# Kernel tuning notes

Measured on AMD Instinct MI355X. Metric: run time of the kernel, lower is better.

The kernel has to match this reference:

```python
import jax, jax.numpy as jnp
import numpy as np

B = 256
D, H, W = 15, 64, 128    # depth, latitude, longitude of input grid
d, h, w = 5, 16, 32      # grid after AveragePooling3D(3,4,4)
L_DEPTH = (d + 2) * h * w      # 3584
L_LON   = d * h * (w + 2)      # 2720
L_LAT   = d * (h + 2) * w      # 2880


def _local1d(xp, wt, bias):
    # Unshared-weight LocallyConnected1D(filters=1, kernel=3) + relu.
    # xp: (B, L+2) padded sequence; wt: (L, 3); bias: (L,)
    L = wt.shape[0]
    y = (wt[:, 0] * xp[:, 0:L]
         + wt[:, 1] * xp[:, 1:L + 1]
         + wt[:, 2] * xp[:, 2:L + 2]
         + bias)
    return jax.nn.relu(y)


def setup_inputs() -> dict:
    key = jax.random.key(0)
    ks = jax.random.split(key, 7)
    s = 0.1
    return {
        "x": jax.random.normal(ks[0], (B, D, H, W, 1), jnp.float32),
        "w_depth": jax.random.normal(ks[1], (L_DEPTH, 3), jnp.float32) * s,
        "b_depth": jax.random.normal(ks[2], (L_DEPTH,), jnp.float32) * s,
        "w_lon": jax.random.normal(ks[3], (L_LON, 3), jnp.float32) * s,
        "b_lon": jax.random.normal(ks[4], (L_LON,), jnp.float32) * s,
        "w_lat": jax.random.normal(ks[5], (L_LAT, 3), jnp.float32) * s,
        "b_lat": jax.random.normal(ks[6], (L_LAT,), jnp.float32) * s,
    }


def reference(x, w_depth, b_depth, w_lon, b_lon, w_lat, b_lat):
    Bn = x.shape[0]
    # AveragePooling3D(3,4,4): dims divide evenly -> reshape + mean
    xs = x.reshape(Bn, d, 3, h, 4, w, 4, 1).mean(axis=(2, 4, 6))  # (B,d,h,w,1)

    # ---- depth axis: pad depth, permute (3,2,1,4), flatten, local conv ----
    t = jnp.pad(xs, ((0, 0), (1, 1), (0, 0), (0, 0), (0, 0)))     # (B,d+2,h,w,1)
    t = jnp.transpose(t, (0, 3, 2, 1, 4))                         # (B,w,h,d+2,1)
    t = t.reshape(Bn, L_DEPTH)
    t = jnp.pad(t, ((0, 0), (1, 1)))                              # ZeroPadding1D(1)
    t = _local1d(t, w_depth, b_depth)
    t = t.reshape(Bn, w, h, d + 2, 1)
    t = jnp.transpose(t, (0, 3, 2, 1, 4))                         # (B,d+2,h,w,1)
    t = t[:, 1:-1]                                                # crop depth -> (B,d,h,w,1)

    # ---- longitude axis: pad last spatial dim, identity permute ----
    u = jnp.pad(t, ((0, 0), (0, 0), (0, 0), (1, 1), (0, 0)))      # (B,d,h,w+2,1)
    u = u.reshape(Bn, L_LON)
    u = jnp.pad(u, ((0, 0), (1, 1)))
    u = _local1d(u, w_lon, b_lon)
    u = u.reshape(Bn, d, h, w + 2, 1)
    u = u[:, :, :, 1:-1]                                          # (B,d,h,w,1)

    # ---- latitude axis: pad lat, permute (1,3,2,4) ----
    v = jnp.pad(u, ((0, 0), (0, 0), (1, 1), (0, 0), (0, 0)))      # (B,d,h+2,w,1)
    v = jnp.transpose(v, (0, 1, 3, 2, 4))                         # (B,d,w,h+2,1)
    v = v.reshape(Bn, L_LAT)
    v = jnp.pad(v, ((0, 0), (1, 1)))
    v = _local1d(v, w_lat, b_lat)
    v = v.reshape(Bn, d, w, h + 2, 1)
    v = jnp.transpose(v, (0, 1, 3, 2, 4))                         # (B,d,h+2,w,1)
    v = v[:, :, 1:-1]                                             # (B,d,h,w,1)

    # UpSampling3D(3,4,4): nearest-neighbor repeat
    out = jnp.broadcast_to(
        v[:, :, None, :, None, :, None, :],
        (Bn, d, 3, h, 4, w, 4, 1)
    ).reshape(Bn, D, H, W, 1)
    return out
```

## Files before the change

kernel.cpp:

```cpp
#include <hip/hip_runtime.h>


#define NELEM (15 * 64 * 128)
#define NCELL 2560
#define LD    3584
#define LLON  2720

__global__ __launch_bounds__(256) void k_down(const float* __restrict__ x,
                                              float* __restrict__ ds)
{
    const int b  = blockIdx.y;
    const int c  = blockIdx.x * 256 + threadIdx.x;
    const int iw = c & 31;
    const int ih = (c >> 5) & 15;
    const int id = c >> 9;

    const float* p = x + (size_t)b * NELEM + ((id * 3) * 64 + ih * 4) * 128 + iw * 4;
    float s = 0.f;
    #pragma unroll
    for (int dd = 0; dd < 3; ++dd) {
        #pragma unroll
        for (int hh = 0; hh < 4; ++hh) {
            const float4 v = *reinterpret_cast<const float4*>(p + (dd * 64 + hh) * 128);
            s += (v.x + v.y) + (v.z + v.w);
        }
    }
    ds[(size_t)b * NCELL + c] = s * (1.f / 48.f);
}

__device__ __forceinline__ float tf_depth(const float* __restrict__ dsb, int f)
{
    const int k  = f % 7;
    const int q  = f / 7;
    const int ih = q & 15;
    const int iw = q >> 4;
    return (k >= 1 && k <= 5) ? dsb[((k - 1) * 16 + ih) * 32 + iw] : 0.f;
}

__device__ __forceinline__ float t1_val(const float* __restrict__ dsb,
                                        const float* __restrict__ wd,
                                        const float* __restrict__ bd, int l)
{
    const float x0 = (l > 0)      ? tf_depth(dsb, l - 1) : 0.f;
    const float x1 =                tf_depth(dsb, l);
    const float x2 = (l < LD - 1) ? tf_depth(dsb, l + 1) : 0.f;
    return fmaxf(wd[l * 3] * x0 + wd[l * 3 + 1] * x1 + wd[l * 3 + 2] * x2 + bd[l], 0.f);
}

__device__ __forceinline__ float uf_lon(const float* __restrict__ dsb,
                                        const float* __restrict__ wd,
                                        const float* __restrict__ bd, int f)
{
    const int kw  = f % 34;
    const int q   = f / 34;
    const int ih  = q & 15;
    const int dep = q >> 4;
    if (kw < 1 || kw > 32) return 0.f;
    return t1_val(dsb, wd, bd, ((kw - 1) * 16 + ih) * 7 + dep + 1);
}

__global__ __launch_bounds__(256) void k_mid(const float* __restrict__ ds,
                                             const float* __restrict__ wd,
                                             const float* __restrict__ bd,
                                             const float* __restrict__ wl,
                                             const float* __restrict__ bl,
                                             float* __restrict__ u1)
{
    const int b = blockIdx.y;
    const int m = blockIdx.x * 256 + threadIdx.x;
    if (m >= LLON) return;
    const float* dsb = ds + (size_t)b * NCELL;

    const float x0 = (m > 0)        ? uf_lon(dsb, wd, bd, m - 1) : 0.f;
    const float x1 =                  uf_lon(dsb, wd, bd, m);
    const float x2 = (m < LLON - 1) ? uf_lon(dsb, wd, bd, m + 1) : 0.f;
    const float y  = wl[m * 3] * x0 + wl[m * 3 + 1] * x1 + wl[m * 3 + 2] * x2 + bl[m];
    u1[(size_t)b * LLON + m] = fmaxf(y, 0.f);
}

__device__ __forceinline__ float vf_lat(const float* __restrict__ u1b, int f)
{
    const int kh  = f % 18;
    const int q   = f / 18;
    const int iw  = q & 31;
    const int dep = q >> 5;
    return (kh >= 1 && kh <= 16) ? u1b[(dep * 16 + kh - 1) * 34 + iw + 1] : 0.f;
}

__global__ __launch_bounds__(256) void k_vup(const float* __restrict__ u1,
                                             const float* __restrict__ w,
                                             const float* __restrict__ bias,
                                             float* __restrict__ out)
{
    const int b   = blockIdx.y;
    const int c   = blockIdx.x * 256 + threadIdx.x;
    const int iww = c & 31;
    const int ihh = (c >> 5) & 15;
    const int dep = c >> 9;
    const int n   = (dep * 32 + iww) * 18 + ihh + 1;

    const float* u1b = u1 + (size_t)b * LLON;
    const float x0 = vf_lat(u1b, n - 1);
    const float x1 = vf_lat(u1b, n);
    const float x2 = vf_lat(u1b, n + 1);
    const float y  = fmaxf(w[n * 3] * x0 + w[n * 3 + 1] * x1 + w[n * 3 + 2] * x2 + bias[n], 0.f);
    const float4 y4 = make_float4(y, y, y, y);

    float4* ob = reinterpret_cast<float4*>(out + (size_t)b * NELEM);
    #pragma unroll
    for (int dd = 0; dd < 3; ++dd) {
        #pragma unroll
        for (int hh = 0; hh < 4; ++hh) {
            ob[((dep * 3 + dd) * 64 + ihh * 4 + hh) * 32 + iww] = y4;
        }
    }
}

extern "C" void kernel_launch(void* const* d_in, const int* in_sizes, int n_in,
                              void* d_out, int out_size, void* d_ws, size_t ws_size,
                              hipStream_t stream) {
    const float* x       = (const float*)d_in[0];
    const float* w_depth = (const float*)d_in[1];
    const float* b_depth = (const float*)d_in[2];
    const float* w_lon   = (const float*)d_in[3];
    const float* b_lon   = (const float*)d_in[4];
    const float* w_lat   = (const float*)d_in[5];
    const float* b_lat   = (const float*)d_in[6];
    float* out = (float*)d_out;

    const int Bn = in_sizes[0] / NELEM;

    float* ds = (float*)d_ws;
    float* u1 = ds + (size_t)Bn * NCELL;

    k_down<<<dim3(NCELL / 256, Bn), dim3(256), 0, stream>>>(x, ds);
    k_mid <<<dim3((LLON + 255) / 256, Bn), dim3(256), 0, stream>>>(ds, w_depth, b_depth,
                                                                   w_lon, b_lon, u1);
    k_vup <<<dim3(NCELL / 256, Bn), dim3(256), 0, stream>>>(u1, w_lat, b_lat, out);
}
```

Before: 242.0 us.

## Fuse avg-pool downsample into depth/longitude kernel via per-latitude LDS tile

Merges the pooling kernel and the depth+longitude local-conv kernel into one launch. Each block owns one latitude row for one batch, pools the 5x32 cells into shared memory, then computes the 170 longitude outputs for that row straight from LDS. This is valid because the depth and longitude stages never mix latitude rows. It removes one launch and the global round trip of the pooled array. In exchange only 160 and 170 of the 256 threads do work in each phase, and there are fewer, lighter blocks.

```diff
diff --git a/kernel.cpp b/kernel.cpp
--- a/kernel.cpp
+++ b/kernel.cpp
@@ -6,76 +6,76 @@
 #define LD    3584
 #define LLON  2720
 
-__global__ __launch_bounds__(256) void k_down(const float* __restrict__ x,
-                                              float* __restrict__ ds)
-{
-    const int b  = blockIdx.y;
-    const int c  = blockIdx.x * 256 + threadIdx.x;
-    const int iw = c & 31;
-    const int ih = (c >> 5) & 15;
-    const int id = c >> 9;
-
-    const float* p = x + (size_t)b * NELEM + ((id * 3) * 64 + ih * 4) * 128 + iw * 4;
-    float s = 0.f;
-    #pragma unroll
-    for (int dd = 0; dd < 3; ++dd) {
-        #pragma unroll
-        for (int hh = 0; hh < 4; ++hh) {
-            const float4 v = *reinterpret_cast<const float4*>(p + (dd * 64 + hh) * 128);
-            s += (v.x + v.y) + (v.z + v.w);
-        }
-    }
-    ds[(size_t)b * NCELL + c] = s * (1.f / 48.f);
-}
-
-__device__ __forceinline__ float tf_depth(const float* __restrict__ dsb, int f)
+__device__ __forceinline__ float tf_depth_lds(const float* __restrict__ lds, int f)
 {
     const int k  = f % 7;
     const int q  = f / 7;
-    const int ih = q & 15;
     const int iw = q >> 4;
-    return (k >= 1 && k <= 5) ? dsb[((k - 1) * 16 + ih) * 32 + iw] : 0.f;
+    return (k >= 1 && k <= 5) ? lds[(k - 1) * 32 + iw] : 0.f;
 }
 
-__device__ __forceinline__ float t1_val(const float* __restrict__ dsb,
-                                        const float* __restrict__ wd,
-                                        const float* __restrict__ bd, int l)
+__device__ __forceinline__ float t1_val_lds(const float* __restrict__ lds,
+                                            const float* __restrict__ wd,
+                                            const float* __restrict__ bd, int l)
 {
-    const float x0 = (l > 0)      ? tf_depth(dsb, l - 1) : 0.f;
-    const float x1 =                tf_depth(dsb, l);
-    const float x2 = (l < LD - 1) ? tf_depth(dsb, l + 1) : 0.f;
+    const float x0 = tf_depth_lds(lds, l - 1);
+    const float x1 = tf_depth_lds(lds, l);
+    const float x2 = tf_depth_lds(lds, l + 1);
     return fmaxf(wd[l * 3] * x0 + wd[l * 3 + 1] * x1 + wd[l * 3 + 2] * x2 + bd[l], 0.f);
 }
 
-__device__ __forceinline__ float uf_lon(const float* __restrict__ dsb,
-                                        const float* __restrict__ wd,
-                                        const float* __restrict__ bd, int f)
+__device__ __forceinline__ float uf_lon_lds(const float* __restrict__ lds,
+                                            const float* __restrict__ wd,
+                                            const float* __restrict__ bd,
+                                            int f, int ih)
 {
     const int kw  = f % 34;
-    const int q   = f / 34;
-    const int ih  = q & 15;
-    const int dep = q >> 4;
     if (kw < 1 || kw > 32) return 0.f;
-    return t1_val(dsb, wd, bd, ((kw - 1) * 16 + ih) * 7 + dep + 1);
+    const int dep = (f / 34) >> 4;
+    return t1_val_lds(lds, wd, bd, ((kw - 1) * 16 + ih) * 7 + dep + 1);
 }
 
-__global__ __launch_bounds__(256) void k_mid(const float* __restrict__ ds,
-                                             const float* __restrict__ wd,
-                                             const float* __restrict__ bd,
-                                             const float* __restrict__ wl,
-                                             const float* __restrict__ bl,
-                                             float* __restrict__ u1)
+__global__ __launch_bounds__(256) void k_down_mid(const float* __restrict__ x,
+                                                  const float* __restrict__ wd,
+                                                  const float* __restrict__ bd,
+                                                  const float* __restrict__ wl,
+                                                  const float* __restrict__ bl,
+                                                  float* __restrict__ u1)
 {
-    const int b = blockIdx.y;
-    const int m = blockIdx.x * 256 + threadIdx.x;
-    if (m >= LLON) return;
-    const float* dsb = ds + (size_t)b * NCELL;
+    const int b   = blockIdx.y;
+    const int ih  = blockIdx.x;
+    const int tid = threadIdx.x;
 
-    const float x0 = (m > 0)        ? uf_lon(dsb, wd, bd, m - 1) : 0.f;
-    const float x1 =                  uf_lon(dsb, wd, bd, m);
-    const float x2 = (m < LLON - 1) ? uf_lon(dsb, wd, bd, m + 1) : 0.f;
-    const float y  = wl[m * 3] * x0 + wl[m * 3 + 1] * x1 + wl[m * 3 + 2] * x2 + bl[m];
-    u1[(size_t)b * LLON + m] = fmaxf(y, 0.f);
+    __shared__ float ds[5 * 32];
+
+    if (tid < 160) {
+        const int iw = tid & 31;
+        const int id = tid >> 5;
+        const float* p = x + (size_t)b * NELEM + ((id * 3) * 64 + ih * 4) * 128 + iw * 4;
+        float s = 0.f;
+        #pragma unroll
+        for (int dd = 0; dd < 3; ++dd) {
+            #pragma unroll
+            for (int hh = 0; hh < 4; ++hh) {
+                const float4 v = *reinterpret_cast<const float4*>(p + (dd * 64 + hh) * 128);
+                s += (v.x + v.y) + (v.z + v.w);
+            }
+        }
+        ds[id * 32 + iw] = s * (1.f / 48.f);
+    }
+    __syncthreads();
+
+    if (tid < 170) {
+        const int kw  = tid % 34;
+        const int dep = tid / 34;
+        const int m   = (dep * 16 + ih) * 34 + kw;
+
+        const float x0 = (m > 0)        ? uf_lon_lds(ds, wd, bd, m - 1, ih) : 0.f;
+        const float x1 =                  uf_lon_lds(ds, wd, bd, m,     ih);
+        const float x2 = (m < LLON - 1) ? uf_lon_lds(ds, wd, bd, m + 1, ih) : 0.f;
+        const float y  = wl[m * 3] * x0 + wl[m * 3 + 1] * x1 + wl[m * 3 + 2] * x2 + bl[m];
+        u1[(size_t)b * LLON + m] = fmaxf(y, 0.f);
+    }
 }
 
 __device__ __forceinline__ float vf_lat(const float* __restrict__ u1b, int f)
@@ -130,11 +130,9 @@
 
     const int Bn = in_sizes[0] / NELEM;
 
-    float* ds = (float*)d_ws;
-    float* u1 = ds + (size_t)Bn * NCELL;
+    float* u1 = (float*)d_ws;
 
-    k_down<<<dim3(NCELL / 256, Bn), dim3(256), 0, stream>>>(x, ds);
-    k_mid <<<dim3((LLON + 255) / 256, Bn), dim3(256), 0, stream>>>(ds, w_depth, b_depth,
-                                                                   w_lon, b_lon, u1);
-    k_vup <<<dim3(NCELL / 256, Bn), dim3(256), 0, stream>>>(u1, w_lat, b_lat, out);
+    k_down_mid<<<dim3(16, Bn), dim3(256), 0, stream>>>(x, w_depth, b_depth,
+                                                       w_lon, b_lon, u1);
+    k_vup     <<<dim3(NCELL / 256, Bn), dim3(256), 0, stream>>>(u1, w_lat, b_lat, out);
 }
```

New measurement: 231.1 us. -4.5%, faster.

## Fuse depth, longitude and latitude stages into one per-depth-slice kernel

Applied to the files above, without the earlier changes.

Replaces the k_mid and k_vup kernels with a single k_rest kernel. Each block handles one batch item and one depth slice, stages three neighbouring depth slices of the pooled grid in shared memory, computes the depth and longitude local convolutions, keeps the longitude result in LDS, then applies the latitude convolution and writes the upsampled output. This removes one kernel launch, the u1 global round-trip and the recomputation of depth values, at the cost of redundant depth-stencil work across neighbouring iw and two block-level syncs.

```diff
diff --git a/kernel.cpp b/kernel.cpp
--- a/kernel.cpp
+++ b/kernel.cpp
@@ -3,8 +3,6 @@
 
 #define NELEM (15 * 64 * 128)
 #define NCELL 2560
-#define LD    3584
-#define LLON  2720
 
 __global__ __launch_bounds__(256) void k_down(const float* __restrict__ x,
                                               float* __restrict__ ds)
@@ -28,90 +26,76 @@
     ds[(size_t)b * NCELL + c] = s * (1.f / 48.f);
 }
 
-__device__ __forceinline__ float tf_depth(const float* __restrict__ dsb, int f)
-{
-    const int k  = f % 7;
-    const int q  = f / 7;
-    const int ih = q & 15;
-    const int iw = q >> 4;
-    return (k >= 1 && k <= 5) ? dsb[((k - 1) * 16 + ih) * 32 + iw] : 0.f;
-}
-
-__device__ __forceinline__ float t1_val(const float* __restrict__ dsb,
-                                        const float* __restrict__ wd,
-                                        const float* __restrict__ bd, int l)
-{
-    const float x0 = (l > 0)      ? tf_depth(dsb, l - 1) : 0.f;
-    const float x1 =                tf_depth(dsb, l);
-    const float x2 = (l < LD - 1) ? tf_depth(dsb, l + 1) : 0.f;
-    return fmaxf(wd[l * 3] * x0 + wd[l * 3 + 1] * x1 + wd[l * 3 + 2] * x2 + bd[l], 0.f);
-}
-
-__device__ __forceinline__ float uf_lon(const float* __restrict__ dsb,
-                                        const float* __restrict__ wd,
-                                        const float* __restrict__ bd, int f)
-{
-    const int kw  = f % 34;
-    const int q   = f / 34;
-    const int ih  = q & 15;
-    const int dep = q >> 4;
-    if (kw < 1 || kw > 32) return 0.f;
-    return t1_val(dsb, wd, bd, ((kw - 1) * 16 + ih) * 7 + dep + 1);
-}
-
-__global__ __launch_bounds__(256) void k_mid(const float* __restrict__ ds,
-                                             const float* __restrict__ wd,
-                                             const float* __restrict__ bd,
-                                             const float* __restrict__ wl,
-                                             const float* __restrict__ bl,
-                                             float* __restrict__ u1)
-{
-    const int b = blockIdx.y;
-    const int m = blockIdx.x * 256 + threadIdx.x;
-    if (m >= LLON) return;
-    const float* dsb = ds + (size_t)b * NCELL;
-
-    const float x0 = (m > 0)        ? uf_lon(dsb, wd, bd, m - 1) : 0.f;
-    const float x1 =                  uf_lon(dsb, wd, bd, m);
-    const float x2 = (m < LLON - 1) ? uf_lon(dsb, wd, bd, m + 1) : 0.f;
-    const float y  = wl[m * 3] * x0 + wl[m * 3 + 1] * x1 + wl[m * 3 + 2] * x2 + bl[m];
-    u1[(size_t)b * LLON + m] = fmaxf(y, 0.f);
-}
-
-__device__ __forceinline__ float vf_lat(const float* __restrict__ u1b, int f)
-{
-    const int kh  = f % 18;
-    const int q   = f / 18;
-    const int iw  = q & 31;
-    const int dep = q >> 5;
-    return (kh >= 1 && kh <= 16) ? u1b[(dep * 16 + kh - 1) * 34 + iw + 1] : 0.f;
-}
-
-__global__ __launch_bounds__(256) void k_vup(const float* __restrict__ u1,
-                                             const float* __restrict__ w,
-                                             const float* __restrict__ bias,
-                                             float* __restrict__ out)
+__global__ __launch_bounds__(512) void k_rest(const float* __restrict__ ds,
+                                              const float* __restrict__ wd,
+                                              const float* __restrict__ bd,
+                                              const float* __restrict__ wl,
+                                              const float* __restrict__ bl,
+                                              const float* __restrict__ wv,
+                                              const float* __restrict__ bv,
+                                              float* __restrict__ out)
 {
     const int b   = blockIdx.y;
-    const int c   = blockIdx.x * 256 + threadIdx.x;
-    const int iww = c & 31;
-    const int ihh = (c >> 5) & 15;
-    const int dep = c >> 9;
-    const int n   = (dep * 32 + iww) * 18 + ihh + 1;
+    const int dep = blockIdx.x;
+    const int tid = threadIdx.x;
 
-    const float* u1b = u1 + (size_t)b * LLON;
-    const float x0 = vf_lat(u1b, n - 1);
-    const float x1 = vf_lat(u1b, n);
-    const float x2 = vf_lat(u1b, n + 1);
-    const float y  = fmaxf(w[n * 3] * x0 + w[n * 3 + 1] * x1 + w[n * 3 + 2] * x2 + bias[n], 0.f);
-    const float4 y4 = make_float4(y, y, y, y);
+    __shared__ float ds3[3 * 512];
+    __shared__ float u_lds[512];
 
-    float4* ob = reinterpret_cast<float4*>(out + (size_t)b * NELEM);
-    #pragma unroll
-    for (int dd = 0; dd < 3; ++dd) {
+    for (int i = tid; i < 3 * 512; i += 512) {
+        const int kp = i >> 9;
+        const int r  = i & 511;
+        const int id = dep - 1 + kp;
+        ds3[i] = (id >= 0 && id <= 4) ? ds[(size_t)b * NCELL + id * 512 + r] : 0.f;
+    }
+    __syncthreads();
+
+    {
+        const int ih = tid >> 5;
+        const int iw = tid & 31;
+        const float* dsr = ds3 + ih * 32;
+
+        auto t1local = [&](int iwq) -> float {
+            const int l = (iwq * 16 + ih) * 7 + dep + 1;
+            const float y = wd[l * 3 + 0] * dsr[iwq]
+                          + wd[l * 3 + 1] * dsr[512 + iwq]
+                          + wd[l * 3 + 2] * dsr[1024 + iwq]
+                          + bd[l];
+            return fmaxf(y, 0.f);
+        };
+        auto ulon = [&](int kwq) -> float {
+            return (kwq >= 1 && kwq <= 32) ? t1local(kwq - 1) : 0.f;
+        };
+
+        const int kw = iw + 1;
+        const int m  = (dep * 16 + ih) * 34 + kw;
+        const float y = wl[m * 3 + 0] * ulon(kw - 1)
+                      + wl[m * 3 + 1] * ulon(kw)
+                      + wl[m * 3 + 2] * ulon(kw + 1)
+                      + bl[m];
+        u_lds[tid] = fmaxf(y, 0.f);
+    }
+    __syncthreads();
+
+    {
+        const int ihh = tid >> 5;
+        const int iww = tid & 31;
+        const int n   = (dep * 32 + iww) * 18 + ihh + 1;
+
+        const float x0 = (ihh > 0)  ? u_lds[(ihh - 1) * 32 + iww] : 0.f;
+        const float x1 =              u_lds[ihh * 32 + iww];
+        const float x2 = (ihh < 15) ? u_lds[(ihh + 1) * 32 + iww] : 0.f;
+        const float y  = fmaxf(wv[n * 3 + 0] * x0 + wv[n * 3 + 1] * x1
+                             + wv[n * 3 + 2] * x2 + bv[n], 0.f);
+        const float4 y4 = make_float4(y, y, y, y);
+
+        float4* ob = reinterpret_cast<float4*>(out + (size_t)b * NELEM);
         #pragma unroll
-        for (int hh = 0; hh < 4; ++hh) {
-            ob[((dep * 3 + dd) * 64 + ihh * 4 + hh) * 32 + iww] = y4;
+        for (int dd = 0; dd < 3; ++dd) {
+            #pragma unroll
+            for (int hh = 0; hh < 4; ++hh) {
+                ob[((dep * 3 + dd) * 64 + ihh * 4 + hh) * 32 + iww] = y4;
+            }
         }
     }
 }
@@ -131,10 +115,8 @@
     const int Bn = in_sizes[0] / NELEM;
 
     float* ds = (float*)d_ws;
-    float* u1 = ds + (size_t)Bn * NCELL;
 
     k_down<<<dim3(NCELL / 256, Bn), dim3(256), 0, stream>>>(x, ds);
-    k_mid <<<dim3((LLON + 255) / 256, Bn), dim3(256), 0, stream>>>(ds, w_depth, b_depth,
-                                                                   w_lon, b_lon, u1);
-    k_vup <<<dim3(NCELL / 256, Bn), dim3(256), 0, stream>>>(u1, w_lat, b_lat, out);
+    k_rest<<<dim3(5, Bn), dim3(512), 0, stream>>>(ds, w_depth, b_depth,
+                                                  w_lon, b_lon, w_lat, b_lat, out);
 }
```

Measured after the change: 231.4 us. -4.4%, faster.
